# Kernel tuning notes

Measured on AMD Instinct MI355X. Metric: run time of the kernel, lower is better.

## Reference

```python
import jax, jax.numpy as jnp
import numpy as np

B, S, DIM = 2, 2048, 768
HEADS, HEAD_DIM = 12, 64
WINDOW = 512
LEVELS, EXP = 4, 4
LR = 0.1
LN_EPS = 1e-5


def layernorm(x, g, b):
    m = jnp.mean(x, axis=-1, keepdims=True)
    v = jnp.mean(jnp.square(x - m), axis=-1, keepdims=True)
    return (x - m) * jax.lax.rsqrt(v + LN_EPS) * g + b


def setup_inputs() -> dict:
    key = jax.random.key(0)
    ks = jax.random.split(key, 12)
    D = DIM
    w = lambda k, shape: jax.random.normal(k, shape, jnp.float32) * 0.02
    return {
        "x": jax.random.normal(ks[0], (B, S, D), jnp.float32),
        # nn.MultiheadAttention params (packed qkv in_proj + out_proj)
        "in_proj_w": w(ks[1], (3 * D, D)),
        "in_proj_b": jnp.zeros((3 * D,), jnp.float32),
        "out_proj_w": w(ks[2], (D, D)),
        "out_proj_b": jnp.zeros((D,), jnp.float32),
        "ln_local_g": jnp.ones((D,), jnp.float32),
        "ln_local_b": jnp.zeros((D,), jnp.float32),
        # SelfModifyingTitans (delta-rule linear memory) params
        "t_wq": w(ks[3], (HEADS * HEAD_DIM, D)),
        "t_wk": w(ks[4], (HEADS * HEAD_DIM, D)),
        "t_wv": w(ks[5], (HEADS * HEAD_DIM, D)),
        "t_wo": w(ks[6], (D, HEADS * HEAD_DIM)),
        "ln_tit_g": jnp.ones((D,), jnp.float32),
        "ln_tit_b": jnp.zeros((D,), jnp.float32),
        # combine gate
        "gate_w": w(ks[7], (D, 2 * D)),
        "gate_b": jnp.zeros((D,), jnp.float32),
        # ContinuumMemorySystem: LEVELS stacked FFNs dim -> EXP*dim -> dim
        "cms_w1": w(ks[8], (LEVELS, EXP * D, D)),
        "cms_b1": jnp.zeros((LEVELS, EXP * D), jnp.float32),
        "cms_w2": w(ks[9], (LEVELS, D, EXP * D)),
        "cms_b2": jnp.zeros((LEVELS, D), jnp.float32),
        "ln_cms_g": jnp.ones((D,), jnp.float32),
        "ln_cms_b": jnp.zeros((D,), jnp.float32),
    }


def reference(x, in_proj_w, in_proj_b, out_proj_w, out_proj_b, ln_local_g,
              ln_local_b, t_wq, t_wk, t_wv, t_wo, ln_tit_g, ln_tit_b,
              gate_w, gate_b, cms_w1, cms_b1, cms_w2, cms_b2,
              ln_cms_g, ln_cms_b):
    Bq, Sq, D = x.shape
    H, dh = HEADS, D // HEADS

    # ---- causal sliding-window MHA (mask True = blocked in torch; here keep allowed) ----
    i = jnp.arange(Sq)[:, None]
    j = jnp.arange(Sq)[None, :]
    allowed = (j <= i) & (j > i - WINDOW)  # [S, S]

    qkv = x @ in_proj_w.T + in_proj_b  # [B,S,3D]
    q, k, v = jnp.split(qkv, 3, axis=-1)
    split_heads = lambda t: t.reshape(Bq, Sq, H, dh).transpose(0, 2, 1, 3)
    q, k, v = split_heads(q), split_heads(k), split_heads(v)
    scale = 1.0 / np.sqrt(dh).astype(np.float32)
    scores = jnp.einsum('bhqd,bhkd->bhqk', q * scale, k)
    scores = jnp.where(allowed, scores, jnp.finfo(scores.dtype).min)
    attn = jax.nn.softmax(scores, axis=-1)
    o = jnp.einsum('bhqk,bhkd->bhqd', attn, v)
    local_out = o.transpose(0, 2, 1, 3).reshape(Bq, Sq, D) @ out_proj_w.T + out_proj_b
    x_local = layernorm(x + local_out, ln_local_g, ln_local_b)

    # ---- SelfModifyingTitans: delta-rule recurrent associative memory ----
    tq = (x @ t_wq.T).reshape(Bq, Sq, HEADS, HEAD_DIM).transpose(1, 0, 2, 3)  # [S,B,H,dh]
    tk = (x @ t_wk.T).reshape(Bq, Sq, HEADS, HEAD_DIM).transpose(1, 0, 2, 3)
    tv = (x @ t_wv.T).reshape(Bq, Sq, HEADS, HEAD_DIM).transpose(1, 0, 2, 3)

    def step(M, qkv_t):
        qt, kt, vt = qkv_t  # each [B,H,dh]
        pred = jnp.einsum('bhde,bhd->bhe', M, kt)
        M = M + LR * jnp.einsum('bhd,bhe->bhde', kt, vt - pred)  # delta rule
        ot = jnp.einsum('bhde,bhd->bhe', M, qt)
        return M, ot

    M0 = jnp.zeros((Bq, HEADS, HEAD_DIM, HEAD_DIM), x.dtype)
    memory_state, os_seq = jax.lax.scan(step, M0, (tq, tk, tv))
    titans_out = os_seq.transpose(1, 0, 2, 3).reshape(Bq, Sq, HEADS * HEAD_DIM) @ t_wo.T
    x_global = layernorm(x + titans_out, ln_tit_g, ln_tit_b)

    # ---- gated combine ----
    gate = jax.nn.sigmoid(jnp.concatenate([x_local, x_global], axis=-1) @ gate_w.T + gate_b)
    xc = gate * x_local + (1.0 - gate) * x_global

    # ---- ContinuumMemorySystem: average of LEVELS FFNs ----
    h = jnp.einsum('bsd,lfd->blsf', xc, cms_w1) + cms_b1[None, :, None, :]
    h = jax.nn.gelu(h)
    cms = jnp.einsum('blsf,ldf->blsd', h, cms_w2) + cms_b2[None, :, None, :]
    cms_out = cms.mean(axis=1)

    out = layernorm(xc + cms_out, ln_cms_g, ln_cms_b)
    return out, memory_state
```

## Files before the change

### kernel.cpp

```cpp
#include <hip/hip_runtime.h>
#include <hip/hip_bf16.h>
#include <math.h>

typedef unsigned short u16;
typedef __attribute__((ext_vector_type(8))) short bf8v;
typedef __attribute__((ext_vector_type(4))) short bf4v;
typedef __attribute__((ext_vector_type(4))) float f4v;

__device__ __forceinline__ float bf2f(u16 h) {
    unsigned int u = ((unsigned int)h) << 16;
    float f;
    __builtin_memcpy(&f, &u, 4);
    return f;
}
__device__ __forceinline__ u16 f2bf(float f) {
    unsigned int u;
    __builtin_memcpy(&u, &f, 4);
    unsigned int r = (u + 0x7FFFu + ((u >> 16) & 1u)) >> 16;
    return (u16)r;
}
__device__ __forceinline__ float gelu_tanh(float x) {
    float x3 = x * x * x;
    float y = 0.7978845608028654f * (x + 0.044715f * x3);
    float e = __expf(2.f * y);
    float t = 1.f - 2.f / (e + 1.f);
    return 0.5f * x * (1.f + t);
}

#define SEQ 2048
#define DIMC 768
#define NHEAD 12
#define QKVC 2304
#define LRc 0.1f

__global__ __launch_bounds__(256) void cast_f2b_kernel(
    const float* __restrict__ src, u16* __restrict__ dst, int n)
{
    int i = (blockIdx.x * 256 + threadIdx.x) * 4;
    if (i + 3 < n) {
        float4 v = *(const float4*)(src + i);
        dst[i + 0] = f2bf(v.x);
        dst[i + 1] = f2bf(v.y);
        dst[i + 2] = f2bf(v.z);
        dst[i + 3] = f2bf(v.w);
    }
}

__global__ __launch_bounds__(256) void cast_split_kernel(
    const float* __restrict__ src, u16* __restrict__ hi, u16* __restrict__ lo, int n)
{
    int i = (blockIdx.x * 256 + threadIdx.x) * 4;
    if (i + 3 < n) {
        float4 v = *(const float4*)(src + i);
        float vv[4] = {v.x, v.y, v.z, v.w};
        #pragma unroll
        for (int j = 0; j < 4; ++j) {
            u16 h = f2bf(vv[j]);
            hi[i + j] = h;
            lo[i + j] = f2bf(vv[j] - bf2f(h));
        }
    }
}

__global__ __launch_bounds__(256) void gemm128_kernel(
    const u16* __restrict__ A, const u16* __restrict__ W,
    const float* __restrict__ bias, u16* __restrict__ outb, float* __restrict__ outf,
    int M, int N, int K, int act, int mode, float oscale)
{
    __shared__ u16 As[128 * 32];
    __shared__ u16 Bs[128 * 32];
    const int tid  = threadIdx.x;
    const int lane = tid & 63;
    const int wv   = tid >> 6;
    const int r16  = lane & 15;
    const int quad = lane >> 4;
    const int mh   = (wv & 1) * 64;
    const int nh   = (wv >> 1) * 64;
    const int m_blk = blockIdx.x * 128;
    const int n_blk = blockIdx.y * 128;

    const int c0 = tid, c1 = tid + 256;
    const u16* Ag0 = A + (size_t)(m_blk + (c0 >> 2)) * K + (c0 & 3) * 8;
    const u16* Ag1 = A + (size_t)(m_blk + (c1 >> 2)) * K + (c1 & 3) * 8;
    const u16* Wg0 = W + (size_t)(n_blk + (c0 >> 2)) * K + (c0 & 3) * 8;
    const u16* Wg1 = W + (size_t)(n_blk + (c1 >> 2)) * K + (c1 & 3) * 8;
    u16* As0 = As + c0 * 8;
    u16* As1 = As + c1 * 8;
    u16* Bs0 = Bs + c0 * 8;
    u16* Bs1 = Bs + c1 * 8;

    f4v acc[4][4];
    #pragma unroll
    for (int i = 0; i < 4; ++i)
        #pragma unroll
        for (int j = 0; j < 4; ++j) acc[i][j] = (f4v){0.f, 0.f, 0.f, 0.f};

    bf8v av0 = *(const bf8v*)Ag0;
    bf8v av1 = *(const bf8v*)Ag1;
    bf8v bv0 = *(const bf8v*)Wg0;
    bf8v bv1 = *(const bf8v*)Wg1;
    for (int k0 = 0; k0 < K; k0 += 32) {
        __syncthreads();
        *(bf8v*)As0 = av0;
        *(bf8v*)As1 = av1;
        *(bf8v*)Bs0 = bv0;
        *(bf8v*)Bs1 = bv1;
        __syncthreads();
        if (k0 + 32 < K) {
            av0 = *(const bf8v*)(Ag0 + k0 + 32);
            av1 = *(const bf8v*)(Ag1 + k0 + 32);
            bv0 = *(const bf8v*)(Wg0 + k0 + 32);
            bv1 = *(const bf8v*)(Wg1 + k0 + 32);
        }
        bf8v af[4], bfj[4];
        #pragma unroll
        for (int i = 0; i < 4; ++i)
            af[i] = *(const bf8v*)(As + (mh + i * 16 + r16) * 32 + quad * 8);
        #pragma unroll
        for (int j = 0; j < 4; ++j)
            bfj[j] = *(const bf8v*)(Bs + (nh + j * 16 + r16) * 32 + quad * 8);
        #pragma unroll
        for (int i = 0; i < 4; ++i)
            #pragma unroll
            for (int j = 0; j < 4; ++j)
                acc[i][j] = __builtin_amdgcn_mfma_f32_16x16x32_bf16(af[i], bfj[j], acc[i][j], 0, 0, 0);
    }

    #pragma unroll
    for (int j = 0; j < 4; ++j) {
        int gn = n_blk + nh + j * 16 + r16;
        float bvv = bias ? bias[gn] : 0.f;
        #pragma unroll
        for (int i = 0; i < 4; ++i) {
            #pragma unroll
            for (int rr = 0; rr < 4; ++rr) {
                int gm = m_blk + mh + i * 16 + quad * 4 + rr;
                float v = acc[i][j][rr] + bvv;
                if (act == 1) v = gelu_tanh(v);
                else if (act == 2) v = 1.f / (1.f + __expf(-v));
                size_t oi = (size_t)gm * N + gn;
                if (mode == 0) outb[oi] = f2bf(v);
                else if (mode == 1) outf[oi] = oscale * v;
                else outf[oi] += oscale * v;
            }
        }
    }
}

__global__ __launch_bounds__(256) void gemm_split_kernel(
    const u16* __restrict__ Ahi, const u16* __restrict__ Alo,
    const u16* __restrict__ Whi, const u16* __restrict__ Wlo,
    float* __restrict__ outf, int M, int N, int K)
{
    const int lane = threadIdx.x & 63;
    const int wv   = threadIdx.x >> 6;
    const int m0   = blockIdx.x * 64 + wv * 16;
    const int n0   = blockIdx.y * 64;
    const int r16  = lane & 15;
    const int quad = lane >> 4;

    const size_t arow = (size_t)(m0 + r16) * K + quad * 8;
    const size_t wrow = (size_t)(n0 + r16) * K + quad * 8;
    const size_t wstride = (size_t)16 * K;

    f4v acc[4];
    #pragma unroll
    for (int j = 0; j < 4; ++j) acc[j] = (f4v){0.f, 0.f, 0.f, 0.f};

    for (int k0 = 0; k0 < K; k0 += 32) {
        bf8v ah = *(const bf8v*)(Ahi + arow + k0);
        bf8v al = *(const bf8v*)(Alo + arow + k0);
        #pragma unroll
        for (int j = 0; j < 4; ++j) {
            bf8v bh = *(const bf8v*)(Whi + wrow + j * wstride + k0);
            bf8v bl = *(const bf8v*)(Wlo + wrow + j * wstride + k0);
            acc[j] = __builtin_amdgcn_mfma_f32_16x16x32_bf16(ah, bh, acc[j], 0, 0, 0);
            acc[j] = __builtin_amdgcn_mfma_f32_16x16x32_bf16(ah, bl, acc[j], 0, 0, 0);
            acc[j] = __builtin_amdgcn_mfma_f32_16x16x32_bf16(al, bh, acc[j], 0, 0, 0);
        }
    }

    #pragma unroll
    for (int j = 0; j < 4; ++j) {
        int gn = n0 + j * 16 + r16;
        #pragma unroll
        for (int rr = 0; rr < 4; ++rr) {
            int gm = m0 + quad * 4 + rr;
            outf[(size_t)gm * N + gn] = acc[j][rr];
        }
    }
}

#define NJ 527
#define NJP 548
__global__ __launch_bounds__(256) void attn_kernel(
    const u16* __restrict__ qkv, u16* __restrict__ outp)
{
    const int bh = blockIdx.y;
    const int b = bh / NHEAD, h = bh % NHEAD;
    const int q0 = blockIdx.x * 16;
    const int jbase = q0 - 511;
    const int tid = threadIdx.x;
    const int lane = tid & 63;
    const int wv = tid >> 6;
    const int r16 = lane & 15;
    const int quad = lane >> 4;

    __shared__ float ss[16][NJP];
    __shared__ float redbuf[16][17];
    __shared__ float rowmax[16];
    __shared__ float rowinv[16];

    const size_t qrow = (size_t)(b * SEQ + q0 + r16) * QKVC + h * 64 + quad * 8;
    bf8v qf0 = *(const bf8v*)(qkv + qrow);
    bf8v qf1 = *(const bf8v*)(qkv + qrow + 32);

    for (int jt = wv; jt < 33; jt += 4) {
        int js_l = jt * 16 + r16;
        int j = jbase + js_l;
        int jc = j & (SEQ - 1);
        const u16* kp = qkv + (size_t)(b * SEQ + jc) * QKVC + DIMC + h * 64 + quad * 8;
        bf8v kf0 = *(const bf8v*)kp;
        bf8v kf1 = *(const bf8v*)(kp + 32);
        f4v acc = (f4v){0.f, 0.f, 0.f, 0.f};
        acc = __builtin_amdgcn_mfma_f32_16x16x32_bf16(qf0, kf0, acc, 0, 0, 0);
        acc = __builtin_amdgcn_mfma_f32_16x16x32_bf16(qf1, kf1, acc, 0, 0, 0);
        if (js_l < NJ) {
            #pragma unroll
            for (int rr = 0; rr < 4; ++rr) {
                int row = quad * 4 + rr;
                bool ok = (j >= 0) && (js_l >= row) && (js_l <= row + 511);
                ss[row][js_l] = ok ? 0.125f * acc[rr] : -1e30f;
            }
        }
    }
    for (int t = tid; t < 16 * 17; t += 256)
        ss[t / 17][527 + t % 17] = 0.f;
    __syncthreads();

    {
        int r = tid >> 4, l16 = tid & 15;
        float mx = -1e30f;
        #pragma unroll 1
        for (int js = l16; js < NJ; js += 16) mx = fmaxf(mx, ss[r][js]);
        redbuf[r][l16] = mx;
        __syncthreads();
        if (l16 == 0) {
            float m = -1e30f;
            #pragma unroll
            for (int i = 0; i < 16; ++i) m = fmaxf(m, redbuf[r][i]);
            rowmax[r] = m;
        }
        __syncthreads();
        float rm = rowmax[r];
        float sm = 0.f;
        #pragma unroll 1
        for (int js = l16; js < NJ; js += 16) {
            float p = __expf(ss[r][js] - rm);
            ss[r][js] = p;
            sm += p;
        }
        redbuf[r][l16] = sm;
        __syncthreads();
        if (l16 == 0) {
            float s = 0.f;
            #pragma unroll
            for (int i = 0; i < 16; ++i) s += redbuf[r][i];
            rowinv[r] = 1.f / s;
        }
        __syncthreads();
    }

    {
        const int d0 = wv * 16;
        const u16* vp = qkv + (size_t)b * SEQ * QKVC + 2 * DIMC + h * 64 + d0 + r16;
        f4v oacc = (f4v){0.f, 0.f, 0.f, 0.f};
        for (int k0 = 0; k0 < 544; k0 += 32) {
            float4 p0 = *(const float4*)&ss[r16][k0 + quad * 8];
            float4 p1 = *(const float4*)&ss[r16][k0 + quad * 8 + 4];
            bf8v pa;
            pa[0] = (short)f2bf(p0.x); pa[1] = (short)f2bf(p0.y);
            pa[2] = (short)f2bf(p0.z); pa[3] = (short)f2bf(p0.w);
            pa[4] = (short)f2bf(p1.x); pa[5] = (short)f2bf(p1.y);
            pa[6] = (short)f2bf(p1.z); pa[7] = (short)f2bf(p1.w);
            bf8v vb;
            #pragma unroll
            for (int m = 0; m < 8; ++m) {
                int j = jbase + k0 + quad * 8 + m;
                int jc = j & (SEQ - 1);
                vb[m] = (short)vp[(size_t)jc * QKVC];
            }
            oacc = __builtin_amdgcn_mfma_f32_16x16x32_bf16(pa, vb, oacc, 0, 0, 0);
        }
        #pragma unroll
        for (int rr = 0; rr < 4; ++rr) {
            int row = quad * 4 + rr;
            size_t oi = (size_t)(b * SEQ + q0 + row) * DIMC + h * 64 + d0 + r16;
            outp[oi] = f2bf(oacc[rr] * rowinv[row]);
        }
    }
}

__global__ __launch_bounds__(256) void ln_res_kernel(
    const void* __restrict__ xv, int xf32, const void* __restrict__ yv, int yf32,
    const float* __restrict__ g, const float* __restrict__ be,
    u16* __restrict__ outb, float* __restrict__ outf, int ldout)
{
    const int row = blockIdx.x;
    const int t = threadIdx.x;
    const size_t base = (size_t)row * DIMC;
    float vv[3];
    float s = 0.f, s2 = 0.f;
    #pragma unroll
    for (int i = 0; i < 3; ++i) {
        int d = t + i * 256;
        float a = xf32 ? ((const float*)xv)[base + d] : bf2f(((const u16*)xv)[base + d]);
        float y = yf32 ? ((const float*)yv)[base + d] : bf2f(((const u16*)yv)[base + d]);
        float w = a + y;
        vv[i] = w;
        s += w;
        s2 += w * w;
    }
    #pragma unroll
    for (int o = 32; o > 0; o >>= 1) {
        s  += __shfl_down(s, o);
        s2 += __shfl_down(s2, o);
    }
    __shared__ float rs[4], rq[4], mb[2];
    if ((t & 63) == 0) { rs[t >> 6] = s; rq[t >> 6] = s2; }
    __syncthreads();
    if (t == 0) {
        float S1 = rs[0] + rs[1] + rs[2] + rs[3];
        float S2 = rq[0] + rq[1] + rq[2] + rq[3];
        float mean = S1 * (1.f / 768.f);
        float var = S2 * (1.f / 768.f) - mean * mean;
        mb[0] = mean;
        mb[1] = rsqrtf(var + 1e-5f);
    }
    __syncthreads();
    float mean = mb[0], rstd = mb[1];
    #pragma unroll
    for (int i = 0; i < 3; ++i) {
        int d = t + i * 256;
        float v = (vv[i] - mean) * rstd * g[d] + be[d];
        if (outb) outb[(size_t)row * ldout + d] = f2bf(v);
        else      outf[(size_t)row * ldout + d] = v;
    }
}


__global__ __launch_bounds__(64) void scanA_kernel(
    const u16* __restrict__ tq, const float* __restrict__ tk,
    float* __restrict__ Tm, float* __restrict__ Sm)
{
    const int bid = blockIdx.x;
    const int bh = bid >> 5, c = bid & 31;
    const int b = bh / NHEAD, h = bh % NHEAD;
    const int lane = threadIdx.x;

    __shared__ float Ks[64][68];
    __shared__ float As[64][68];
    __shared__ float Ts[64][68];
    __shared__ u16   Qs[64][72];

    const size_t rowb = (size_t)b * SEQ * DIMC + h * 64;
    const int rg = lane >> 4, c4 = (lane & 15) * 4;
    #pragma unroll 4
    for (int i = 0; i < 16; ++i) {
        int row = i * 4 + rg;
        size_t g = rowb + (size_t)(c * 64 + row) * DIMC + c4;
        *(float4*)&Ks[row][c4] = *(const float4*)(tk + g);
        *(bf4v*)&Qs[row][c4]   = *(const bf4v*)(tq + g);
    }
    __syncthreads();

    float4 kr4[16];
    #pragma unroll
    for (int d4 = 0; d4 < 16; ++d4) kr4[d4] = *(float4*)&Ks[lane][d4 * 4];

    for (int t = 0; t < 64; ++t) {
        float a = 0.f;
        #pragma unroll
        for (int d4 = 0; d4 < 16; ++d4) {
            float4 kt = *(float4*)&Ks[t][d4 * 4];
            a += kt.x * kr4[d4].x + kt.y * kr4[d4].y + kt.z * kr4[d4].z + kt.w * kr4[d4].w;
        }
        As[t][lane] = (lane < t) ? LRc * a : 0.f;
    }
    Ts[0][lane] = (lane == 0) ? 1.f : 0.f;
    for (int t = 1; t < 64; ++t) {
        float s = (lane == t) ? 1.f : 0.f;
        for (int tau = 0; tau < t; ++tau)
            s -= As[t][tau] * Ts[tau][lane];
        Ts[t][lane] = s;
    }
    for (int t = 0; t < 64; ++t) {
        float a = 0.f;
        #pragma unroll
        for (int d4 = 0; d4 < 16; ++d4) {
            bf4v qt = *(bf4v*)&Qs[t][d4 * 4];
            a += bf2f((u16)qt[0]) * kr4[d4].x + bf2f((u16)qt[1]) * kr4[d4].y
               + bf2f((u16)qt[2]) * kr4[d4].z + bf2f((u16)qt[3]) * kr4[d4].w;
        }
        As[t][lane] = (lane <= t) ? a : 0.f;
    }
    __syncthreads();
    float* Tg = Tm + (size_t)bid * 4096;
    float* Sg = Sm + (size_t)bid * 4096;
    #pragma unroll 4
    for (int i = 0; i < 16; ++i) {
        int row = i * 4 + rg;
        *(float4*)(Tg + row * 64 + c4) = *(float4*)&Ts[row][c4];
        *(float4*)(Sg + row * 64 + c4) = *(float4*)&As[row][c4];
    }
}

__global__ __launch_bounds__(256) void scanB_kernel(
    const u16* __restrict__ tq, const float* __restrict__ tk, const float* __restrict__ tv,
    const float* __restrict__ Tm, const float* __restrict__ Sm,
    u16* __restrict__ tito, float* __restrict__ mout)
{
    const int bid = blockIdx.x;
    const int bh = bid >> 2, eh = bid & 3;
    const int b = bh / NHEAD, h = bh % NHEAD;
    const int tid = threadIdx.x;
    const int tx = tid & 3;
    const int r  = tid >> 2;
    const int cc4 = tx * 4;
    const int e0 = eh * 16;

    __shared__ float Ms[64][20];
    __shared__ float Ys[64][20];
    __shared__ float Us[64][20];
    __shared__ float XK[64][68];
    __shared__ float XT[64][68];
    __shared__ float XS[64][68];
    __shared__ u16   Qt[64][72];

    const size_t rowb = (size_t)b * SEQ * DIMC + h * 64;

    for (int i = tid; i < 64 * 20; i += 256) (&Ms[0][0])[i] = 0.f;

    const int srow = tid & 63;
    const int scc  = (tid >> 6) * 16;

    for (int ch = 0; ch < 32; ++ch) {
        const size_t crow = rowb + (size_t)ch * 64 * DIMC;
        {
            const float* s = tk + crow + (size_t)srow * DIMC + scc;
            float4 a0 = *(const float4*)(s + 0), a1 = *(const float4*)(s + 4),
                   a2 = *(const float4*)(s + 8), a3 = *(const float4*)(s + 12);
            float av[16] = {a0.x, a0.y, a0.z, a0.w, a1.x, a1.y, a1.z, a1.w,
                            a2.x, a2.y, a2.z, a2.w, a3.x, a3.y, a3.z, a3.w};
            #pragma unroll
            for (int j = 0; j < 16; ++j) XK[scc + j][srow] = av[j];
            const u16* qg = tq + crow + (size_t)srow * DIMC + scc;
            bf8v q0 = *(const bf8v*)(qg), q1 = *(const bf8v*)(qg + 8);
            #pragma unroll
            for (int j = 0; j < 8; ++j) {
                Qt[scc + j][srow]     = (u16)q0[j];
                Qt[scc + 8 + j][srow] = (u16)q1[j];
            }
        }
        __syncthreads();

        const float* tsrc = Tm + ((size_t)(bh * 32 + ch)) * 4096 + (size_t)srow * 64 + scc;
        float4 t0 = *(const float4*)(tsrc + 0), t1 = *(const float4*)(tsrc + 4),
               t2 = *(const float4*)(tsrc + 8), t3 = *(const float4*)(tsrc + 12);
        float4 v0 = *(const float4*)(tv + crow + (size_t)r * DIMC + e0 + cc4);

        float p[4] = {0.f, 0.f, 0.f, 0.f};
        float oa[4] = {0.f, 0.f, 0.f, 0.f};
        #pragma unroll 4
        for (int k = 0; k < 64; ++k) {
            float a = XK[k][r];
            float q = bf2f(Qt[k][r]);
            float4 m = *(float4*)&Ms[k][cc4];
            p[0] += a * m.x; p[1] += a * m.y; p[2] += a * m.z; p[3] += a * m.w;
            oa[0] += q * m.x; oa[1] += q * m.y; oa[2] += q * m.z; oa[3] += q * m.w;
        }
        {
            float av[16] = {t0.x, t0.y, t0.z, t0.w, t1.x, t1.y, t1.z, t1.w,
                            t2.x, t2.y, t2.z, t2.w, t3.x, t3.y, t3.z, t3.w};
            #pragma unroll
            for (int j = 0; j < 16; ++j) XT[scc + j][srow] = av[j];
            Ys[r][cc4 + 0] = LRc * (v0.x - p[0]);
            Ys[r][cc4 + 1] = LRc * (v0.y - p[1]);
            Ys[r][cc4 + 2] = LRc * (v0.z - p[2]);
            Ys[r][cc4 + 3] = LRc * (v0.w - p[3]);
        }
        __syncthreads();

        const float* ssrc = Sm + ((size_t)(bh * 32 + ch)) * 4096 + (size_t)srow * 64 + scc;
        float4 s0 = *(const float4*)(ssrc + 0), s1 = *(const float4*)(ssrc + 4),
               s2 = *(const float4*)(ssrc + 8), s3 = *(const float4*)(ssrc + 12);

        float u[4] = {0.f, 0.f, 0.f, 0.f};
        #pragma unroll 4
        for (int k = 0; k < 64; ++k) {
            float a = XT[k][r];
            float4 bb = *(float4*)&Ys[k][cc4];
            u[0] += a * bb.x; u[1] += a * bb.y; u[2] += a * bb.z; u[3] += a * bb.w;
        }
        {
            float av[16] = {s0.x, s0.y, s0.z, s0.w, s1.x, s1.y, s1.z, s1.w,
                            s2.x, s2.y, s2.z, s2.w, s3.x, s3.y, s3.z, s3.w};
            #pragma unroll
            for (int j = 0; j < 16; ++j) XS[scc + j][srow] = av[j];
            #pragma unroll
            for (int j = 0; j < 4; ++j) Us[r][cc4 + j] = u[j];
        }
        __syncthreads();

        float m0[4];
        #pragma unroll
        for (int j = 0; j < 4; ++j) m0[j] = Ms[r][cc4 + j];
        #pragma unroll 4
        for (int k = 0; k < 64; ++k) {
            float sa = XS[k][r];
            float ka = XK[r][k];
            float4 uu = *(float4*)&Us[k][cc4];
            oa[0] += sa * uu.x; oa[1] += sa * uu.y; oa[2] += sa * uu.z; oa[3] += sa * uu.w;
            m0[0] += ka * uu.x; m0[1] += ka * uu.y; m0[2] += ka * uu.z; m0[3] += ka * uu.w;
        }
        #pragma unroll
        for (int j = 0; j < 4; ++j) Ms[r][cc4 + j] = m0[j];
        {
            u16* op = tito + crow + (size_t)r * DIMC + e0 + cc4;
            bf4v w;
            #pragma unroll
            for (int j = 0; j < 4; ++j) w[j] = (short)f2bf(oa[j]);
            *(bf4v*)op = w;
        }
        __syncthreads();
    }
    {
        float* mg = mout + (size_t)bh * 4096 + (size_t)r * 64 + e0 + cc4;
        *(float4*)mg = *(float4*)&Ms[r][cc4];
    }
}

__global__ __launch_bounds__(768) void combine_kernel(
    const u16* __restrict__ xlg, const u16* __restrict__ gate, u16* __restrict__ xc)
{
    const int row = blockIdx.x;
    const int t = threadIdx.x;
    float g = bf2f(gate[(size_t)row * DIMC + t]);
    float xl = bf2f(xlg[(size_t)row * 1536 + t]);
    float xg = bf2f(xlg[(size_t)row * 1536 + 768 + t]);
    xc[(size_t)row * DIMC + t] = f2bf(g * xl + (1.f - g) * xg);
}

extern "C" void kernel_launch(void* const* d_in, const int* in_sizes, int n_in,
                              void* d_out, int out_size, void* d_ws, size_t ws_size,
                              hipStream_t stream) {
    const float* x          = (const float*)d_in[0];
    const float* in_proj_w  = (const float*)d_in[1];
    const float* in_proj_b  = (const float*)d_in[2];
    const float* out_proj_w = (const float*)d_in[3];
    const float* out_proj_b = (const float*)d_in[4];
    const float* ln_local_g = (const float*)d_in[5];
    const float* ln_local_b = (const float*)d_in[6];
    const float* t_wq       = (const float*)d_in[7];
    const float* t_wk       = (const float*)d_in[8];
    const float* t_wv       = (const float*)d_in[9];
    const float* t_wo       = (const float*)d_in[10];
    const float* ln_tit_g   = (const float*)d_in[11];
    const float* ln_tit_b   = (const float*)d_in[12];
    const float* gate_w     = (const float*)d_in[13];
    const float* gate_b     = (const float*)d_in[14];
    const float* cms_w1     = (const float*)d_in[15];
    const float* cms_b1     = (const float*)d_in[16];
    const float* cms_w2     = (const float*)d_in[17];
    const float* cms_b2     = (const float*)d_in[18];
    const float* ln_cms_g   = (const float*)d_in[19];
    const float* ln_cms_b   = (const float*)d_in[20];

    const int Mrows = 2 * SEQ;

    u16* ws = (u16*)d_ws;
    u16*   qkv   = ws + 0;
    u16*   lout  = ws + 0;
    u16*   gout  = ws + 3145728;
    u16*   gact  = ws + 6291456;
    u16*   tq16  = ws + 9437184;
    u16*   wB    = ws + 9437184;
    u16*   w_inp = ws + 12582912;
    float* tkf   = (float*)(ws + 12582912);
    u16*   W1S   = ws + 12582912;
    u16*   W2S   = ws + 14942208;
    float* tvf   = (float*)(ws + 18874368);
    u16*   w_tqb = ws + 25165824;
    u16*   tito  = ws + 25165824;
    u16*   w_hi  = ws + 28311552;
    u16*   w_lo  = ws + 28901376;
    u16*   attn_o= ws + 28311552;
    u16*   xc    = ws + 28311552;
    u16*   x_hi  = ws + 31457280;
    u16*   x_lo  = ws + 34603008;
    u16*   xlg   = ws + 31457280;
    u16*   h     = ws + 0;

    float* out32 = (float*)d_out;
    float* cmsacc = out32;
    float* mout  = out32 + (size_t)Mrows * DIMC;

    float* Tmat = (float*)(ws + 31457280);
    float* Smat = out32;

    auto cast = [&](const float* src, u16* dst, int n) {
        cast_f2b_kernel<<<(n + 1023) / 1024, 256, 0, stream>>>(src, dst, n);
    };
    auto gemm = [&](const u16* A, const u16* W, const float* bias, u16* ob, float* of,
                    int M, int N, int K, int act, int mode, float oscale) {
        gemm128_kernel<<<dim3(M / 128, N / 128), 256, 0, stream>>>(
            A, W, bias, ob, of, M, N, K, act, mode, oscale);
    };
    auto split = [&](const float* src, u16* hi, u16* lo, int n) {
        cast_split_kernel<<<(n + 1023) / 1024, 256, 0, stream>>>(src, hi, lo, n);
    };

    split(x, x_hi, x_lo, Mrows * DIMC);
    cast(in_proj_w, w_inp, QKVC * DIMC);
    gemm(x_hi, w_inp, in_proj_b, qkv, nullptr, Mrows, QKVC, DIMC, 0, 0, 0.f);
    split(t_wk, w_hi, w_lo, DIMC * DIMC);
    gemm_split_kernel<<<dim3(Mrows / 64, DIMC / 64), 256, 0, stream>>>(
        x_hi, x_lo, w_hi, w_lo, tkf, Mrows, DIMC, DIMC);
    split(t_wv, w_hi, w_lo, DIMC * DIMC);
    gemm_split_kernel<<<dim3(Mrows / 64, DIMC / 64), 256, 0, stream>>>(
        x_hi, x_lo, w_hi, w_lo, tvf, Mrows, DIMC, DIMC);
    cast(t_wq, w_tqb, DIMC * DIMC);
    gemm(x_hi, w_tqb, nullptr, tq16, nullptr, Mrows, DIMC, DIMC, 0, 0, 0.f);
    attn_kernel<<<dim3(SEQ / 16, 2 * NHEAD), 256, 0, stream>>>(qkv, attn_o);
    scanA_kernel<<<24 * 32, 64, 0, stream>>>(tq16, tkf, Tmat, Smat);
    scanB_kernel<<<24 * 4, 256, 0, stream>>>(tq16, tkf, tvf, Tmat, Smat, tito, mout);
    cast(out_proj_w, wB, DIMC * DIMC);
    gemm(attn_o, wB, out_proj_b, lout, nullptr, Mrows, DIMC, DIMC, 0, 0, 0.f);
    ln_res_kernel<<<Mrows, 256, 0, stream>>>(x, 1, lout, 0, ln_local_g, ln_local_b, xlg, nullptr, 1536);
    cast(t_wo, wB, DIMC * DIMC);
    gemm(tito, wB, nullptr, gout, nullptr, Mrows, DIMC, DIMC, 0, 0, 0.f);
    ln_res_kernel<<<Mrows, 256, 0, stream>>>(x, 1, gout, 0, ln_tit_g, ln_tit_b, xlg + 768, nullptr, 1536);
    cast(gate_w, wB, DIMC * 2 * DIMC);
    gemm(xlg, wB, gate_b, gact, nullptr, Mrows, DIMC, 2 * DIMC, 2, 0, 0.f);
    combine_kernel<<<Mrows, 768, 0, stream>>>(xlg, gact, xc);
    for (int l = 0; l < 4; ++l) {
        cast(cms_w1 + (size_t)l * 2359296, W1S, 2359296);
        cast(cms_w2 + (size_t)l * 2359296, W2S, 2359296);
        gemm(xc, W1S, cms_b1 + l * 3072, h, nullptr, Mrows, 3072, DIMC, 1, 0, 0.f);
        gemm(h, W2S, cms_b2 + l * DIMC, nullptr, cmsacc, Mrows, DIMC, 3072, 0, l == 0 ? 1 : 2, 0.25f);
    }
    ln_res_kernel<<<Mrows, 256, 0, stream>>>(xc, 0, cmsacc, 1, ln_cms_g, ln_cms_b, nullptr, out32, DIMC);

    (void)in_sizes; (void)n_in; (void)out_size; (void)ws_size;
}
```

Measured before the change: 1.354 ms.

## Batch independent GEMMs, casts and layernorms via grid z; split-K the CMS down-projection

```diff
diff --git a/kernel.cpp b/kernel.cpp
--- a/kernel.cpp
+++ b/kernel.cpp
@@ -46,6 +46,22 @@
     }
 }
 
+__global__ __launch_bounds__(256) void cast2_f2b_kernel(
+    const float* __restrict__ s0, u16* __restrict__ d0,
+    const float* __restrict__ s1, u16* __restrict__ d1, int n)
+{
+    const float* s = blockIdx.z ? s1 : s0;
+    u16* d = blockIdx.z ? d1 : d0;
+    int i = (blockIdx.x * 256 + threadIdx.x) * 4;
+    if (i + 3 < n) {
+        float4 v = *(const float4*)(s + i);
+        d[i + 0] = f2bf(v.x);
+        d[i + 1] = f2bf(v.y);
+        d[i + 2] = f2bf(v.z);
+        d[i + 3] = f2bf(v.w);
+    }
+}
+
 __global__ __launch_bounds__(256) void cast_split_kernel(
     const float* __restrict__ src, u16* __restrict__ hi, u16* __restrict__ lo, int n)
 {
@@ -62,10 +78,10 @@
     }
 }
 
-__global__ __launch_bounds__(256) void gemm128_kernel(
+__device__ __forceinline__ void gemm128_body(
     const u16* __restrict__ A, const u16* __restrict__ W,
     const float* __restrict__ bias, u16* __restrict__ outb, float* __restrict__ outf,
-    int M, int N, int K, int act, int mode, float oscale)
+    int N, int Kloop, int Kstride, int act, int mode, float oscale)
 {
     __shared__ u16 As[128 * 32];
     __shared__ u16 Bs[128 * 32];
@@ -80,10 +96,10 @@
     const int n_blk = blockIdx.y * 128;
 
     const int c0 = tid, c1 = tid + 256;
-    const u16* Ag0 = A + (size_t)(m_blk + (c0 >> 2)) * K + (c0 & 3) * 8;
-    const u16* Ag1 = A + (size_t)(m_blk + (c1 >> 2)) * K + (c1 & 3) * 8;
-    const u16* Wg0 = W + (size_t)(n_blk + (c0 >> 2)) * K + (c0 & 3) * 8;
-    const u16* Wg1 = W + (size_t)(n_blk + (c1 >> 2)) * K + (c1 & 3) * 8;
+    const u16* Ag0 = A + (size_t)(m_blk + (c0 >> 2)) * Kstride + (c0 & 3) * 8;
+    const u16* Ag1 = A + (size_t)(m_blk + (c1 >> 2)) * Kstride + (c1 & 3) * 8;
+    const u16* Wg0 = W + (size_t)(n_blk + (c0 >> 2)) * Kstride + (c0 & 3) * 8;
+    const u16* Wg1 = W + (size_t)(n_blk + (c1 >> 2)) * Kstride + (c1 & 3) * 8;
     u16* As0 = As + c0 * 8;
     u16* As1 = As + c1 * 8;
     u16* Bs0 = Bs + c0 * 8;
@@ -99,14 +115,14 @@
     bf8v av1 = *(const bf8v*)Ag1;
     bf8v bv0 = *(const bf8v*)Wg0;
     bf8v bv1 = *(const bf8v*)Wg1;
-    for (int k0 = 0; k0 < K; k0 += 32) {
+    for (int k0 = 0; k0 < Kloop; k0 += 32) {
         __syncthreads();
         *(bf8v*)As0 = av0;
         *(bf8v*)As1 = av1;
         *(bf8v*)Bs0 = bv0;
         *(bf8v*)Bs1 = bv1;
         __syncthreads();
-        if (k0 + 32 < K) {
+        if (k0 + 32 < Kloop) {
             av0 = *(const bf8v*)(Ag0 + k0 + 32);
             av1 = *(const bf8v*)(Ag1 + k0 + 32);
             bv0 = *(const bf8v*)(Wg0 + k0 + 32);
@@ -141,17 +157,52 @@
                 size_t oi = (size_t)gm * N + gn;
                 if (mode == 0) outb[oi] = f2bf(v);
                 else if (mode == 1) outf[oi] = oscale * v;
-                else outf[oi] += oscale * v;
+                else if (mode == 2) outf[oi] += oscale * v;
+                else atomicAdd(outf + oi, oscale * v);
             }
         }
     }
+}
+
+__global__ __launch_bounds__(256) void gemm128_kernel(
+    const u16* __restrict__ A, const u16* __restrict__ W,
+    const float* __restrict__ bias, u16* __restrict__ outb, float* __restrict__ outf,
+    int N, int K, int act, int mode, float oscale)
+{
+    gemm128_body(A, W, bias, outb, outf, N, K, K, act, mode, oscale);
+}
+
+__global__ __launch_bounds__(256) void gemm128_dual_kernel(
+    const u16* __restrict__ A0, const u16* __restrict__ W0,
+    const float* __restrict__ b0, u16* __restrict__ o0,
+    const u16* __restrict__ A1, const u16* __restrict__ W1,
+    const float* __restrict__ b1, u16* __restrict__ o1,
+    int N, int K)
+{
+    if (blockIdx.z == 0) gemm128_body(A0, W0, b0, o0, nullptr, N, K, K, 0, 0, 0.f);
+    else                 gemm128_body(A1, W1, b1, o1, nullptr, N, K, K, 0, 0, 0.f);
+}
+
+__global__ __launch_bounds__(256) void gemm128_ksplit_kernel(
+    const u16* __restrict__ A, const u16* __restrict__ W,
+    const float* __restrict__ bias, float* __restrict__ outf,
+    int N, int Kstride, int KC, float oscale)
+{
+    const int z = blockIdx.z;
+    gemm128_body(A + (size_t)z * KC, W + (size_t)z * KC, z == 0 ? bias : nullptr,
+                 nullptr, outf, N, KC, Kstride, 0, 3, oscale);
 }
 
 __global__ __launch_bounds__(256) void gemm_split_kernel(
     const u16* __restrict__ Ahi, const u16* __restrict__ Alo,
-    const u16* __restrict__ Whi, const u16* __restrict__ Wlo,
-    float* __restrict__ outf, int M, int N, int K)
-{
+    const u16* __restrict__ W0hi, const u16* __restrict__ W0lo, float* __restrict__ out0,
+    const u16* __restrict__ W1hi, const u16* __restrict__ W1lo, float* __restrict__ out1,
+    int M, int N, int K)
+{
+    const u16* Whi = blockIdx.z ? W1hi : W0hi;
+    const u16* Wlo = blockIdx.z ? W1lo : W0lo;
+    float* outf    = blockIdx.z ? out1 : out0;
+
     const int lane = threadIdx.x & 63;
     const int wv   = threadIdx.x >> 6;
     const int m0   = blockIdx.x * 64 + wv * 16;
@@ -348,6 +399,54 @@
     }
 }
 
+__global__ __launch_bounds__(256) void ln_res2_kernel(
+    const float* __restrict__ x,
+    const u16* __restrict__ y0, const float* __restrict__ g0, const float* __restrict__ b0,
+    u16* __restrict__ o0,
+    const u16* __restrict__ y1, const float* __restrict__ g1, const float* __restrict__ b1,
+    u16* __restrict__ o1, int M)
+{
+    int row = blockIdx.x;
+    const u16* y; const float* g; const float* be; u16* ob;
+    if (row < M) { y = y0; g = g0; be = b0; ob = o0; }
+    else { row -= M; y = y1; g = g1; be = b1; ob = o1; }
+    const int t = threadIdx.x;
+    const size_t base = (size_t)row * DIMC;
+    float vv[3];
+    float s = 0.f, s2 = 0.f;
+    #pragma unroll
+    for (int i = 0; i < 3; ++i) {
+        int d = t + i * 256;
+        float w = x[base + d] + bf2f(y[base + d]);
+        vv[i] = w;
+        s += w;
+        s2 += w * w;
+    }
+    #pragma unroll
+    for (int o = 32; o > 0; o >>= 1) {
+        s  += __shfl_down(s, o);
+        s2 += __shfl_down(s2, o);
+    }
+    __shared__ float rs[4], rq[4], mb[2];
+    if ((t & 63) == 0) { rs[t >> 6] = s; rq[t >> 6] = s2; }
+    __syncthreads();
+    if (t == 0) {
+        float S1 = rs[0] + rs[1] + rs[2] + rs[3];
+        float S2 = rq[0] + rq[1] + rq[2] + rq[3];
+        float mean = S1 * (1.f / 768.f);
+        float var = S2 * (1.f / 768.f) - mean * mean;
+        mb[0] = mean;
+        mb[1] = rsqrtf(var + 1e-5f);
+    }
+    __syncthreads();
+    float mean = mb[0], rstd = mb[1];
+    #pragma unroll
+    for (int i = 0; i < 3; ++i) {
+        int d = t + i * 256;
+        float v = (vv[i] - mean) * rstd * g[d] + be[d];
+        ob[(size_t)row * 1536 + d] = f2bf(v);
+    }
+}
 
 __global__ __launch_bounds__(64) void scanA_kernel(
     const u16* __restrict__ tq, const float* __restrict__ tk,
@@ -585,6 +684,7 @@
     u16*   gact  = ws + 6291456;
     u16*   tq16  = ws + 9437184;
     u16*   wB    = ws + 9437184;
+    u16*   wB2   = ws + 10027008;
     u16*   w_inp = ws + 12582912;
     float* tkf   = (float*)(ws + 12582912);
     u16*   W1S   = ws + 12582912;
@@ -594,6 +694,8 @@
     u16*   tito  = ws + 25165824;
     u16*   w_hi  = ws + 28311552;
     u16*   w_lo  = ws + 28901376;
+    u16*   w_hi2 = ws + 29491200;
+    u16*   w_lo2 = ws + 30081024;
     u16*   attn_o= ws + 28311552;
     u16*   xc    = ws + 28311552;
     u16*   x_hi  = ws + 31457280;
@@ -614,7 +716,7 @@
     auto gemm = [&](const u16* A, const u16* W, const float* bias, u16* ob, float* of,
                     int M, int N, int K, int act, int mode, float oscale) {
         gemm128_kernel<<<dim3(M / 128, N / 128), 256, 0, stream>>>(
-            A, W, bias, ob, of, M, N, K, act, mode, oscale);
+            A, W, bias, ob, of, N, K, act, mode, oscale);
     };
     auto split = [&](const float* src, u16* hi, u16* lo, int n) {
         cast_split_kernel<<<(n + 1023) / 1024, 256, 0, stream>>>(src, hi, lo, n);
@@ -624,30 +726,31 @@
     cast(in_proj_w, w_inp, QKVC * DIMC);
     gemm(x_hi, w_inp, in_proj_b, qkv, nullptr, Mrows, QKVC, DIMC, 0, 0, 0.f);
     split(t_wk, w_hi, w_lo, DIMC * DIMC);
-    gemm_split_kernel<<<dim3(Mrows / 64, DIMC / 64), 256, 0, stream>>>(
-        x_hi, x_lo, w_hi, w_lo, tkf, Mrows, DIMC, DIMC);
-    split(t_wv, w_hi, w_lo, DIMC * DIMC);
-    gemm_split_kernel<<<dim3(Mrows / 64, DIMC / 64), 256, 0, stream>>>(
-        x_hi, x_lo, w_hi, w_lo, tvf, Mrows, DIMC, DIMC);
+    split(t_wv, w_hi2, w_lo2, DIMC * DIMC);
+    gemm_split_kernel<<<dim3(Mrows / 64, DIMC / 64, 2), 256, 0, stream>>>(
+        x_hi, x_lo, w_hi, w_lo, tkf, w_hi2, w_lo2, tvf, Mrows, DIMC, DIMC);
     cast(t_wq, w_tqb, DIMC * DIMC);
     gemm(x_hi, w_tqb, nullptr, tq16, nullptr, Mrows, DIMC, DIMC, 0, 0, 0.f);
     attn_kernel<<<dim3(SEQ / 16, 2 * NHEAD), 256, 0, stream>>>(qkv, attn_o);
     scanA_kernel<<<24 * 32, 64, 0, stream>>>(tq16, tkf, Tmat, Smat);
     scanB_kernel<<<24 * 4, 256, 0, stream>>>(tq16, tkf, tvf, Tmat, Smat, tito, mout);
-    cast(out_proj_w, wB, DIMC * DIMC);
-    gemm(attn_o, wB, out_proj_b, lout, nullptr, Mrows, DIMC, DIMC, 0, 0, 0.f);
-    ln_res_kernel<<<Mrows, 256, 0, stream>>>(x, 1, lout, 0, ln_local_g, ln_local_b, xlg, nullptr, 1536);
-    cast(t_wo, wB, DIMC * DIMC);
-    gemm(tito, wB, nullptr, gout, nullptr, Mrows, DIMC, DIMC, 0, 0, 0.f);
-    ln_res_kernel<<<Mrows, 256, 0, stream>>>(x, 1, gout, 0, ln_tit_g, ln_tit_b, xlg + 768, nullptr, 1536);
+    cast2_f2b_kernel<<<dim3((DIMC * DIMC + 1023) / 1024, 1, 2), 256, 0, stream>>>(
+        out_proj_w, wB, t_wo, wB2, DIMC * DIMC);
+    gemm128_dual_kernel<<<dim3(Mrows / 128, DIMC / 128, 2), 256, 0, stream>>>(
+        attn_o, wB, out_proj_b, lout, tito, wB2, nullptr, gout, DIMC, DIMC);
+    ln_res2_kernel<<<2 * Mrows, 256, 0, stream>>>(
+        x, lout, ln_local_g, ln_local_b, xlg,
+        gout, ln_tit_g, ln_tit_b, xlg + 768, Mrows);
     cast(gate_w, wB, DIMC * 2 * DIMC);
     gemm(xlg, wB, gate_b, gact, nullptr, Mrows, DIMC, 2 * DIMC, 2, 0, 0.f);
     combine_kernel<<<Mrows, 768, 0, stream>>>(xlg, gact, xc);
+    hipMemsetAsync(cmsacc, 0, (size_t)Mrows * DIMC * sizeof(float), stream);
     for (int l = 0; l < 4; ++l) {
-        cast(cms_w1 + (size_t)l * 2359296, W1S, 2359296);
-        cast(cms_w2 + (size_t)l * 2359296, W2S, 2359296);
+        cast2_f2b_kernel<<<dim3((2359296 + 1023) / 1024, 1, 2), 256, 0, stream>>>(
+            cms_w1 + (size_t)l * 2359296, W1S, cms_w2 + (size_t)l * 2359296, W2S, 2359296);
         gemm(xc, W1S, cms_b1 + l * 3072, h, nullptr, Mrows, 3072, DIMC, 1, 0, 0.f);
-        gemm(h, W2S, cms_b2 + l * DIMC, nullptr, cmsacc, Mrows, DIMC, 3072, 0, l == 0 ? 1 : 2, 0.25f);
+        gemm128_ksplit_kernel<<<dim3(Mrows / 128, DIMC / 128, 4), 256, 0, stream>>>(
+            h, W2S, cms_b2 + l * DIMC, cmsacc, DIMC, 3072, 768, 0.25f);
     }
     ln_res_kernel<<<Mrows, 256, 0, stream>>>(xc, 0, cmsacc, 1, ln_cms_g, ln_cms_b, nullptr, out32, DIMC);
 
```

Measured after the change: 1.298 ms. -4.2%, faster.
